# Kernel tuning notes

Hardware: AMD Instinct MI355X
Metric: run time of the kernel (lower is better)

The kernel has to match this reference:

```python
import jax, jax.numpy as jnp
from jax import lax
import numpy as np

N, E, G, CPG = 4096, 16, 14, 8  # wafers, experts, groups (wafer sub-arrays), channels per group
C = G * CPG  # 112


def setup_inputs() -> dict:
    key = jax.random.key(0)
    ks = jax.random.split(key, 9)
    s = 0.05
    x = jax.random.normal(ks[0], (N, G, 8, 8), jnp.float32)
    keys = jax.random.randint(ks[1], (N,), 0, E)
    # hexagonal wafer conv mask (buffer in the torch module); corners zeroed
    conv_mask = jnp.array([[1.0, 1.0, 0.0], [1.0, 1.0, 1.0], [0.0, 1.0, 1.0]], jnp.float32)
    enc_conv_w = jax.random.normal(ks[2], (E, C, 1, 3, 3), jnp.float32) * s
    enc_dense_w = jax.random.normal(ks[3], (E, G, 8, 128), jnp.float32) * s
    enc_dense_b = jax.random.normal(ks[4], (E, G, 8), jnp.float32) * s
    dec_dense_w = jax.random.normal(ks[5], (E, G, 128, 8), jnp.float32) * s
    dec_dense_b = jax.random.normal(ks[6], (E, G, 128), jnp.float32) * s
    dec_tconv_w = jax.random.normal(ks[7], (E, C, 1, 3, 3), jnp.float32) * s
    dec_tconv_b = jax.random.normal(ks[8], (E, G), jnp.float32) * s
    return dict(x=x, keys=keys, conv_mask=conv_mask,
                enc_conv_w=enc_conv_w, enc_dense_w=enc_dense_w, enc_dense_b=enc_dense_b,
                dec_dense_w=dec_dense_w, dec_dense_b=dec_dense_b,
                dec_tconv_w=dec_tconv_w, dec_tconv_b=dec_tconv_b)


def reference(x, keys, conv_mask, enc_conv_w, enc_dense_w, enc_dense_b,
              dec_dense_w, dec_dense_b, dec_tconv_w, dec_tconv_b):
    n = x.shape[0]
    dn = ('NCHW', 'OIHW', 'NCHW')

    # ---- encoder: masked grouped conv (bias=False) ----
    wc = enc_conv_w[keys] * conv_mask  # [N,112,1,3,3]; mask broadcasts over spatial taps

    def enc_conv(xi, wi):
        return lax.conv_general_dilated(xi[None], wi, (1, 1), 'SAME',
                                        feature_group_count=G, dimension_numbers=dn)[0]

    h = jax.nn.relu(jax.vmap(enc_conv)(x, wc))           # [N,112,8,8]
    h = h.reshape(n, C, 4, 2, 4, 2).max(axis=(3, 5))     # MaxPool2d(2) -> [N,112,4,4]
    feat = h.reshape(n, G, CPG * 16)                      # [N,14,128] (group-major, matches torch view)
    z = jax.nn.relu(jnp.einsum('ngof,ngf->ngo', enc_dense_w[keys], feat) + enc_dense_b[keys])  # [N,14,8]

    # ---- decoder ----
    y = jax.nn.relu(jnp.einsum('ngfo,ngo->ngf', dec_dense_w[keys], z) + dec_dense_b[keys])  # [N,14,128]
    y = y.reshape(n, C, 4, 4)

    # ConvTranspose2d(112,14,3,stride=2,pad=1,outpad=1,groups=14) as a dilated forward conv
    # with spatially flipped kernels: per group, 8 in -> 1 out.
    wt = jnp.flip(dec_tconv_w[keys].reshape(n, G, CPG, 3, 3), axis=(-2, -1))  # [N,14,8,3,3] OIHW
    bt = dec_tconv_b[keys]  # [N,14]

    def dec_tconv(yi, wi, bi):
        o = lax.conv_general_dilated(yi[None], wi, (1, 1), ((1, 2), (1, 2)),
                                     lhs_dilation=(2, 2), feature_group_count=G,
                                     dimension_numbers=dn)[0]
        return o + bi[:, None, None]

    out = jax.vmap(dec_tconv)(y, wt, bt)  # [N,14,8,8]
    return jax.nn.relu(out)
```

## Files before the change

kernel.cpp:

```cpp
#include <hip/hip_runtime.h>
#include <hip/hip_fp16.h>

#define NG 14
#define NE 16
#define NW 32
#define YW 152

typedef __fp16 h2 __attribute__((ext_vector_type(2)));
typedef __fp16 h4 __attribute__((ext_vector_type(4)));
typedef __fp16 h8 __attribute__((ext_vector_type(8)));

__device__ __forceinline__ float hdot4(h4 a, h4 b, float c) {
    const h2 a0 = __builtin_shufflevector(a, a, 0, 1);
    const h2 a1 = __builtin_shufflevector(a, a, 2, 3);
    const h2 b0 = __builtin_shufflevector(b, b, 0, 1);
    const h2 b1 = __builtin_shufflevector(b, b, 2, 3);
    return __builtin_amdgcn_fdot2(a1, b1, __builtin_amdgcn_fdot2(a0, b0, c, false), false);
}

__global__ __launch_bounds__(1024) void bin_kernel(const int* __restrict__ keys, int N,
                                                   int NBW, int* __restrict__ sorted) {
    __shared__ int hist[NE], offs[NE], cur[NE];
    __shared__ int runTot;
    const int t = threadIdx.x;
    if (t < NE) { hist[t] = 0; cur[t] = 0; }
    __syncthreads();
    for (int i = t; i < N; i += 1024) atomicAdd(&hist[keys[i]], 1);
    __syncthreads();
    if (t == 0) {
        int run = 0;
        for (int e = 0; e < NE; ++e) { offs[e] = run; run += (hist[e] + NW - 1) & ~(NW - 1); }
        runTot = run;
    }
    __syncthreads();
    for (int i = t; i < N; i += 1024) {
        const int e = keys[i];
        sorted[offs[e] + atomicAdd(&cur[e], 1)] = i;
    }
    {
        const int e = t >> 6, l = t & 63;
        const int cnt = hist[e];
        const int padded = (cnt + NW - 1) & ~(NW - 1);
        if (l < padded - cnt) sorted[offs[e] + cnt + l] = -1;
    }
    for (int i = runTot + t; i < NBW; i += 1024) sorted[i] = -1;
}

#define LOADROW(dst, R) do {                                  \
    const float4 a_ = *(const float4*)(xg + (R) * 8);         \
    const float4 b_ = *(const float4*)(xg + (R) * 8 + 4);     \
    dst[0]=0.f; dst[9]=0.f;                                   \
    dst[1]=a_.x; dst[2]=a_.y; dst[3]=a_.z; dst[4]=a_.w;       \
    dst[5]=b_.x; dst[6]=b_.y; dst[7]=b_.z; dst[8]=b_.w;       \
} while (0)

#define CONVGEMV(PR, RM, R0_, R1_, R2_, TZ, BZ)                                \
    {                                                                          \
        float res[4];                                                          \
        _Pragma("unroll")                                                      \
        for (int pc = 0; pc < 4; ++pc) {                                       \
            float mx = 0.f;                                                    \
            _Pragma("unroll")                                                  \
            for (int cl = 0; cl < 2; ++cl) {                                   \
                const int c = 2 * pc + cl;                                     \
                float s0 = w3*R0_[c] + w4*R0_[c+1] + w5*R0_[c+2]               \
                         + w7*R1_[c+1] + w8*R1_[c+2];                          \
                if (!(TZ)) s0 += w0*RM[c] + w1*RM[c+1];                        \
                float s1 = w0*R0_[c] + w1*R0_[c+1]                             \
                         + w3*R1_[c] + w4*R1_[c+1] + w5*R1_[c+2];              \
                if (!(BZ)) s1 += w7*R2_[c+1] + w8*R2_[c+2];                    \
                mx = fmaxf(mx, fmaxf(s0, s1));                                 \
            }                                                                  \
            res[pc] = mx;                                                      \
        }                                                                      \
        const h2 ra = __builtin_amdgcn_cvt_pkrtz(res[0], res[1]);              \
        const h2 rb = __builtin_amdgcn_cvt_pkrtz(res[2], res[3]);              \
        const h2* eb2 = &ews2[((PR) * 8 + ch) * 20];                           \
        _Pragma("unroll")                                                      \
        for (int q = 0; q < 4; ++q) {                                          \
            const h8 v = *(const h8*)(eb2 + q * 4);                            \
            const h2 a0 = __builtin_shufflevector(v, v, 0, 1);                 \
            const h2 a1 = __builtin_shufflevector(v, v, 2, 3);                 \
            const h2 b0 = __builtin_shufflevector(v, v, 4, 5);                 \
            const h2 b1 = __builtin_shufflevector(v, v, 6, 7);                 \
            part[2*q]   = __builtin_amdgcn_fdot2(rb, a1,                       \
                          __builtin_amdgcn_fdot2(ra, a0, part[2*q],   false), false); \
            part[2*q+1] = __builtin_amdgcn_fdot2(rb, b1,                       \
                          __builtin_amdgcn_fdot2(ra, b0, part[2*q+1], false), false); \
        }                                                                      \
    }

__global__ __launch_bounds__(256, 6) void ae_main(
    const float* __restrict__ x,
    const int*   __restrict__ keys,
    const float* __restrict__ conv_mask,
    const float* __restrict__ enc_conv_w,
    const float* __restrict__ enc_dense_w,
    const float* __restrict__ enc_dense_b,
    const float* __restrict__ dec_dense_w,
    const float* __restrict__ dec_dense_b,
    const float* __restrict__ dec_tconv_w,
    const float* __restrict__ dec_tconv_b,
    const int*   __restrict__ sorted,
    float* __restrict__ out)
{
    const int t = threadIdx.x;
    const int chunk = blockIdx.x / NG;
    const int g = blockIdx.x - chunk * NG;

    __shared__ __attribute__((aligned(16))) __half yt[NW * YW];
    __shared__ __attribute__((aligned(16))) h2 ews2[640];
    __shared__ __attribute__((aligned(16))) h2 dws2[512];
    __shared__ __attribute__((aligned(16))) h2 wtr2[48];
    __shared__ __attribute__((aligned(16))) float wcs[72];
    __shared__ float dbs[128];
    __shared__ float ebs[8];

    const int* chunkIds = sorted + chunk * NW;
    const int i0 = chunkIds[0];
    if (i0 < 0) return;
    const int k = keys[i0];

    const int w = t >> 3, ch = t & 7;
    const int idw = chunkIds[w];
    const int idr = (idw < 0) ? i0 : idw;

    const float* xg = x + (size_t)idr * 896 + g * 64;
    float rowA[10], rowB[10], rowC[10], rowD[10], rowE[10];
    LOADROW(rowA, 0);
    LOADROW(rowB, 1);
    LOADROW(rowC, 2);
    LOADROW(rowD, 4);

    const size_t wg1024 = (size_t)(k * NG + g) * 1024;
    {
        const float4 w4_ = *(const float4*)(enc_dense_w + wg1024 + 4 * t);
        const int o = t >> 5, c2 = (t >> 2) & 7, pr = t & 3;
        const int base = (pr * 8 + c2) * 20 + o * 2;
        ews2[base]     = __builtin_amdgcn_cvt_pkrtz(w4_.x, w4_.y);
        ews2[base + 1] = __builtin_amdgcn_cvt_pkrtz(w4_.z, w4_.w);
    }
    if (t < 128) {
        const float4 a = *(const float4*)(dec_dense_w + wg1024 + 8 * t);
        const float4 b = *(const float4*)(dec_dense_w + wg1024 + 8 * t + 4);
        const int c2 = t >> 4, p = t & 15;
        h2* dst = &dws2[(p * 8 + (c2 ^ (p & 7))) * 4];
        dst[0] = __builtin_amdgcn_cvt_pkrtz(a.x, a.y);
        dst[1] = __builtin_amdgcn_cvt_pkrtz(a.z, a.w);
        dst[2] = __builtin_amdgcn_cvt_pkrtz(b.x, b.y);
        dst[3] = __builtin_amdgcn_cvt_pkrtz(b.z, b.w);
    } else if (t < 200) {
        const int i = t - 128, c2 = i / 9, tap = i - c2 * 9;
        wcs[tap * 8 + c2] = enc_conv_w[(size_t)k * 1008 + (g * 8 + c2) * 9 + tap] * conv_mask[tap];
    } else if (t < 208) {
        ebs[t - 200] = enc_dense_b[(size_t)k * 112 + g * 8 + (t - 200)];
    } else if (t < 256) {
        const int i = t - 208, tap = i >> 2, j = i & 3;
        h2 v = (h2)(__fp16)0.f;
        if (tap < 9) {
            const float wa = dec_tconv_w[(size_t)k * 1008 + (g * 8 + 2*j) * 9 + tap];
            const float wb = dec_tconv_w[(size_t)k * 1008 + (g * 8 + 2*j + 1) * 9 + tap];
            v = __builtin_amdgcn_cvt_pkrtz(wa, wb);
        }
        wtr2[tap * 4 + j] = v;
    }
    if (t < 128) {
        dbs[(t & 15) * 8 + (t >> 4)] = dec_dense_b[(size_t)k * 1792 + g * 128 + t];
    }
    __syncthreads();

    const float w0 = wcs[0*8+ch], w1 = wcs[1*8+ch], w3 = wcs[3*8+ch], w4 = wcs[4*8+ch],
                w5 = wcs[5*8+ch], w7 = wcs[7*8+ch], w8 = wcs[8*8+ch];
    float part[8] = {0.f,0.f,0.f,0.f,0.f,0.f,0.f,0.f};

    CONVGEMV(0, rowA, rowA, rowB, rowC, 1, 0);
    LOADROW(rowE, 3);
    CONVGEMV(1, rowB, rowC, rowE, rowD, 0, 0);
    LOADROW(rowA, 5);
    LOADROW(rowB, 6);
    CONVGEMV(2, rowE, rowD, rowA, rowB, 0, 0);
    LOADROW(rowC, 7);
    CONVGEMV(3, rowA, rowB, rowC, rowC, 0, 1);

    float z[8];
    #pragma unroll
    for (int o = 0; o < 8; ++o) {
        float v = part[o];
        v += __shfl_xor(v, 1);
        v += __shfl_xor(v, 2);
        v += __shfl_xor(v, 4);
        z[o] = fmaxf(v + ebs[o], 0.f);
    }
    const h2 z01 = __builtin_amdgcn_cvt_pkrtz(z[0], z[1]);
    const h2 z23 = __builtin_amdgcn_cvt_pkrtz(z[2], z[3]);
    const h2 z45 = __builtin_amdgcn_cvt_pkrtz(z[4], z[5]);
    const h2 z67 = __builtin_amdgcn_cvt_pkrtz(z[6], z[7]);

    __half* yw_ = yt + w * YW;
    #pragma unroll
    for (int pp = 0; pp < 2; ++pp) {
        const int p = ch + pp * 8;
        const int px = p & 7;
        const float4 db0 = *(const float4*)(dbs + p * 8);
        const float4 db1 = *(const float4*)(dbs + p * 8 + 4);
        const float dbv[8] = {db0.x, db0.y, db0.z, db0.w, db1.x, db1.y, db1.z, db1.w};
        __fp16 yv[8];
        #pragma unroll
        for (int c = 0; c < 8; ++c) {
            const h8 v = *(const h8*)(&dws2[(p * 8 + (c ^ px)) * 4]);
            const h2 v0 = __builtin_shufflevector(v, v, 0, 1);
            const h2 v1 = __builtin_shufflevector(v, v, 2, 3);
            const h2 v2 = __builtin_shufflevector(v, v, 4, 5);
            const h2 v3 = __builtin_shufflevector(v, v, 6, 7);
            float acc = dbv[c];
            acc = __builtin_amdgcn_fdot2(z01, v0, acc, false);
            acc = __builtin_amdgcn_fdot2(z23, v1, acc, false);
            acc = __builtin_amdgcn_fdot2(z45, v2, acc, false);
            acc = __builtin_amdgcn_fdot2(z67, v3, acc, false);
            yv[c ^ px] = (__fp16)fmaxf(acc, 0.f);
        }
        h8 o8;
        #pragma unroll
        for (int c = 0; c < 8; ++c) o8[c] = yv[c ^ px];
        *(h8*)(yw_ + (p >> 2) * 40 + (p & 3) * 8) = o8;
    }
    asm volatile("s_waitcnt lgkmcnt(0)" ::: "memory");

    const int oi = ch;
    int iA, rA, iB, rB;
    if ((oi & 1) == 0) { iA = oi >> 1; rA = 3; iB = 0; rB = 9; }
    else { iA = (oi - 1) >> 1; rA = 6;
           if (oi < 7) { iB = (oi + 1) >> 1; rB = 0; } else { iB = 0; rB = 9; } }
    const float bias = dec_tconv_b[k * NG + g];
    const __fp16* ywh = (const __fp16*)(yt) + w * YW;

    h8 yAv[4], yBv[4];
    #pragma unroll
    for (int j = 0; j < 4; ++j) {
        yAv[j] = *(const h8*)(ywh + iA * 40 + j * 8);
        yBv[j] = *(const h8*)(ywh + iB * 40 + j * 8);
    }
    float acc[8] = {0.f,0.f,0.f,0.f,0.f,0.f,0.f,0.f};
    #pragma unroll
    for (int hc = 0; hc < 2; ++hc) {
        const h4 wA0 = *(const h4*)(wtr2 + (rA + 0) * 4 + hc * 2);
        const h4 wA1 = *(const h4*)(wtr2 + (rA + 1) * 4 + hc * 2);
        const h4 wA2 = *(const h4*)(wtr2 + (rA + 2) * 4 + hc * 2);
        const h4 wB0 = *(const h4*)(wtr2 + (rB + 0) * 4 + hc * 2);
        const h4 wB1 = *(const h4*)(wtr2 + (rB + 1) * 4 + hc * 2);
        const h4 wB2 = *(const h4*)(wtr2 + (rB + 2) * 4 + hc * 2);
        h4 yA[4], yB[4];
        #pragma unroll
        for (int j = 0; j < 4; ++j) {
            yA[j] = hc ? __builtin_shufflevector(yAv[j], yAv[j], 4, 5, 6, 7)
                       : __builtin_shufflevector(yAv[j], yAv[j], 0, 1, 2, 3);
            yB[j] = hc ? __builtin_shufflevector(yBv[j], yBv[j], 4, 5, 6, 7)
                       : __builtin_shufflevector(yBv[j], yBv[j], 0, 1, 2, 3);
        }
        acc[0] = hdot4(wB1, yB[0], hdot4(wA1, yA[0], acc[0]));
        acc[1] = hdot4(wB0, yB[1], hdot4(wB2, yB[0],
                 hdot4(wA0, yA[1], hdot4(wA2, yA[0], acc[1]))));
        acc[2] = hdot4(wB1, yB[1], hdot4(wA1, yA[1], acc[2]));
        acc[3] = hdot4(wB0, yB[2], hdot4(wB2, yB[1],
                 hdot4(wA0, yA[2], hdot4(wA2, yA[1], acc[3]))));
        acc[4] = hdot4(wB1, yB[2], hdot4(wA1, yA[2], acc[4]));
        acc[5] = hdot4(wB0, yB[3], hdot4(wB2, yB[2],
                 hdot4(wA0, yA[3], hdot4(wA2, yA[2], acc[5]))));
        acc[6] = hdot4(wB1, yB[3], hdot4(wA1, yA[3], acc[6]));
        acc[7] = hdot4(wB2, yB[3], hdot4(wA2, yA[3], acc[7]));
    }
    if (idw >= 0) {
        float* og = out + (size_t)idw * 896 + g * 64 + oi * 8;
        *(float4*)(og)     = make_float4(fmaxf(acc[0]+bias,0.f), fmaxf(acc[1]+bias,0.f),
                                         fmaxf(acc[2]+bias,0.f), fmaxf(acc[3]+bias,0.f));
        *(float4*)(og + 4) = make_float4(fmaxf(acc[4]+bias,0.f), fmaxf(acc[5]+bias,0.f),
                                         fmaxf(acc[6]+bias,0.f), fmaxf(acc[7]+bias,0.f));
    }
}

extern "C" void kernel_launch(void* const* d_in, const int* in_sizes, int n_in,
                              void* d_out, int out_size, void* d_ws, size_t ws_size,
                              hipStream_t stream) {
    const float* x            = (const float*)d_in[0];
    const int*   keys         = (const int*)d_in[1];
    const float* conv_mask    = (const float*)d_in[2];
    const float* enc_conv_w   = (const float*)d_in[3];
    const float* enc_dense_w  = (const float*)d_in[4];
    const float* enc_dense_b  = (const float*)d_in[5];
    const float* dec_dense_w  = (const float*)d_in[6];
    const float* dec_dense_b  = (const float*)d_in[7];
    const float* dec_tconv_w  = (const float*)d_in[8];
    const float* dec_tconv_b  = (const float*)d_in[9];
    float* out = (float*)d_out;

    const int N = in_sizes[0] / (NG * 64);
    const int CHUNKS = (N + NE * (NW - 1)) / NW + 1;
    int* sorted = (int*)d_ws;

    bin_kernel<<<1, 1024, 0, stream>>>(keys, N, CHUNKS * NW, sorted);
    ae_main<<<CHUNKS * NG, 256, 0, stream>>>(
        x, keys, conv_mask, enc_conv_w, enc_dense_w, enc_dense_b,
        dec_dense_w, dec_dense_b, dec_tconv_w, dec_tconv_b, sorted, out);
}
```

Baseline: 26.96 us.

## Process two sorted chunks per block and reuse expert weights across them

Each block now handles a pair of consecutive sorted chunks for one group instead of a single chunk, which halves the grid. The per-expert weight staging into shared memory is skipped when the second chunk has the same expert, and a barrier is added only when the expert changes. This is meant to cut redundant weight loads and conversions plus per-block launch and setup overhead. In exchange, the two chunks run one after the other inside a block, so there is less parallelism across the GPU and a longer critical path per block.

```diff
diff --git a/kernel.cpp b/kernel.cpp
--- a/kernel.cpp
+++ b/kernel.cpp
@@ -102,11 +102,12 @@
     const float* __restrict__ dec_tconv_w,
     const float* __restrict__ dec_tconv_b,
     const int*   __restrict__ sorted,
+    const int    CHUNKS,
     float* __restrict__ out)
 {
     const int t = threadIdx.x;
-    const int chunk = blockIdx.x / NG;
-    const int g = blockIdx.x - chunk * NG;
+    const int pair = blockIdx.x / NG;
+    const int g = blockIdx.x - pair * NG;
 
     __shared__ __attribute__((aligned(16))) __half yt[NW * YW];
     __shared__ __attribute__((aligned(16))) h2 ews2[640];
@@ -116,165 +117,175 @@
     __shared__ float dbs[128];
     __shared__ float ebs[8];
 
-    const int* chunkIds = sorted + chunk * NW;
-    const int i0 = chunkIds[0];
-    if (i0 < 0) return;
-    const int k = keys[i0];
-
     const int w = t >> 3, ch = t & 7;
-    const int idw = chunkIds[w];
-    const int idr = (idw < 0) ? i0 : idw;
-
-    const float* xg = x + (size_t)idr * 896 + g * 64;
     float rowA[10], rowB[10], rowC[10], rowD[10], rowE[10];
-    LOADROW(rowA, 0);
-    LOADROW(rowB, 1);
-    LOADROW(rowC, 2);
-    LOADROW(rowD, 4);
-
-    const size_t wg1024 = (size_t)(k * NG + g) * 1024;
-    {
-        const float4 w4_ = *(const float4*)(enc_dense_w + wg1024 + 4 * t);
-        const int o = t >> 5, c2 = (t >> 2) & 7, pr = t & 3;
-        const int base = (pr * 8 + c2) * 20 + o * 2;
-        ews2[base]     = __builtin_amdgcn_cvt_pkrtz(w4_.x, w4_.y);
-        ews2[base + 1] = __builtin_amdgcn_cvt_pkrtz(w4_.z, w4_.w);
-    }
-    if (t < 128) {
-        const float4 a = *(const float4*)(dec_dense_w + wg1024 + 8 * t);
-        const float4 b = *(const float4*)(dec_dense_w + wg1024 + 8 * t + 4);
-        const int c2 = t >> 4, p = t & 15;
-        h2* dst = &dws2[(p * 8 + (c2 ^ (p & 7))) * 4];
-        dst[0] = __builtin_amdgcn_cvt_pkrtz(a.x, a.y);
-        dst[1] = __builtin_amdgcn_cvt_pkrtz(a.z, a.w);
-        dst[2] = __builtin_amdgcn_cvt_pkrtz(b.x, b.y);
-        dst[3] = __builtin_amdgcn_cvt_pkrtz(b.z, b.w);
-    } else if (t < 200) {
-        const int i = t - 128, c2 = i / 9, tap = i - c2 * 9;
-        wcs[tap * 8 + c2] = enc_conv_w[(size_t)k * 1008 + (g * 8 + c2) * 9 + tap] * conv_mask[tap];
-    } else if (t < 208) {
-        ebs[t - 200] = enc_dense_b[(size_t)k * 112 + g * 8 + (t - 200)];
-    } else if (t < 256) {
-        const int i = t - 208, tap = i >> 2, j = i & 3;
-        h2 v = (h2)(__fp16)0.f;
-        if (tap < 9) {
-            const float wa = dec_tconv_w[(size_t)k * 1008 + (g * 8 + 2*j) * 9 + tap];
-            const float wb = dec_tconv_w[(size_t)k * 1008 + (g * 8 + 2*j + 1) * 9 + tap];
-            v = __builtin_amdgcn_cvt_pkrtz(wa, wb);
-        }
-        wtr2[tap * 4 + j] = v;
-    }
-    if (t < 128) {
-        dbs[(t & 15) * 8 + (t >> 4)] = dec_dense_b[(size_t)k * 1792 + g * 128 + t];
-    }
-    __syncthreads();
-
-    const float w0 = wcs[0*8+ch], w1 = wcs[1*8+ch], w3 = wcs[3*8+ch], w4 = wcs[4*8+ch],
-                w5 = wcs[5*8+ch], w7 = wcs[7*8+ch], w8 = wcs[8*8+ch];
-    float part[8] = {0.f,0.f,0.f,0.f,0.f,0.f,0.f,0.f};
-
-    CONVGEMV(0, rowA, rowA, rowB, rowC, 1, 0);
-    LOADROW(rowE, 3);
-    CONVGEMV(1, rowB, rowC, rowE, rowD, 0, 0);
-    LOADROW(rowA, 5);
-    LOADROW(rowB, 6);
-    CONVGEMV(2, rowE, rowD, rowA, rowB, 0, 0);
-    LOADROW(rowC, 7);
-    CONVGEMV(3, rowA, rowB, rowC, rowC, 0, 1);
-
-    float z[8];
-    #pragma unroll
-    for (int o = 0; o < 8; ++o) {
-        float v = part[o];
-        v += __shfl_xor(v, 1);
-        v += __shfl_xor(v, 2);
-        v += __shfl_xor(v, 4);
-        z[o] = fmaxf(v + ebs[o], 0.f);
-    }
-    const h2 z01 = __builtin_amdgcn_cvt_pkrtz(z[0], z[1]);
-    const h2 z23 = __builtin_amdgcn_cvt_pkrtz(z[2], z[3]);
-    const h2 z45 = __builtin_amdgcn_cvt_pkrtz(z[4], z[5]);
-    const h2 z67 = __builtin_amdgcn_cvt_pkrtz(z[6], z[7]);
-
-    __half* yw_ = yt + w * YW;
-    #pragma unroll
-    for (int pp = 0; pp < 2; ++pp) {
-        const int p = ch + pp * 8;
-        const int px = p & 7;
-        const float4 db0 = *(const float4*)(dbs + p * 8);
-        const float4 db1 = *(const float4*)(dbs + p * 8 + 4);
-        const float dbv[8] = {db0.x, db0.y, db0.z, db0.w, db1.x, db1.y, db1.z, db1.w};
-        __fp16 yv[8];
+    int kcur = -1;
+
+    for (int c2 = 0; c2 < 2; ++c2) {
+        const int chunk = pair * 2 + c2;
+        if (chunk >= CHUNKS) break;
+        const int* chunkIds = sorted + chunk * NW;
+        const int i0 = chunkIds[0];
+        if (i0 < 0) break;
+        const int k = keys[i0];
+
+        const int idw = chunkIds[w];
+        const int idr = (idw < 0) ? i0 : idw;
+        const float* xg = x + (size_t)idr * 896 + g * 64;
+
+        LOADROW(rowA, 0);
+        LOADROW(rowB, 1);
+        LOADROW(rowC, 2);
+        LOADROW(rowD, 4);
+
+        if (k != kcur) {
+            if (kcur >= 0) __syncthreads();
+            const size_t wg1024 = (size_t)(k * NG + g) * 1024;
+            {
+                const float4 w4_ = *(const float4*)(enc_dense_w + wg1024 + 4 * t);
+                const int o = t >> 5, cc = (t >> 2) & 7, pr = t & 3;
+                const int base = (pr * 8 + cc) * 20 + o * 2;
+                ews2[base]     = __builtin_amdgcn_cvt_pkrtz(w4_.x, w4_.y);
+                ews2[base + 1] = __builtin_amdgcn_cvt_pkrtz(w4_.z, w4_.w);
+            }
+            if (t < 128) {
+                const float4 a = *(const float4*)(dec_dense_w + wg1024 + 8 * t);
+                const float4 b = *(const float4*)(dec_dense_w + wg1024 + 8 * t + 4);
+                const int cc = t >> 4, p = t & 15;
+                h2* dst = &dws2[(p * 8 + (cc ^ (p & 7))) * 4];
+                dst[0] = __builtin_amdgcn_cvt_pkrtz(a.x, a.y);
+                dst[1] = __builtin_amdgcn_cvt_pkrtz(a.z, a.w);
+                dst[2] = __builtin_amdgcn_cvt_pkrtz(b.x, b.y);
+                dst[3] = __builtin_amdgcn_cvt_pkrtz(b.z, b.w);
+            } else if (t < 200) {
+                const int i = t - 128, cc = i / 9, tap = i - cc * 9;
+                wcs[tap * 8 + cc] = enc_conv_w[(size_t)k * 1008 + (g * 8 + cc) * 9 + tap] * conv_mask[tap];
+            } else if (t < 208) {
+                ebs[t - 200] = enc_dense_b[(size_t)k * 112 + g * 8 + (t - 200)];
+            } else if (t < 256) {
+                const int i = t - 208, tap = i >> 2, j = i & 3;
+                h2 v = (h2)(__fp16)0.f;
+                if (tap < 9) {
+                    const float wa = dec_tconv_w[(size_t)k * 1008 + (g * 8 + 2*j) * 9 + tap];
+                    const float wb = dec_tconv_w[(size_t)k * 1008 + (g * 8 + 2*j + 1) * 9 + tap];
+                    v = __builtin_amdgcn_cvt_pkrtz(wa, wb);
+                }
+                wtr2[tap * 4 + j] = v;
+            }
+            if (t < 128) {
+                dbs[(t & 15) * 8 + (t >> 4)] = dec_dense_b[(size_t)k * 1792 + g * 128 + t];
+            }
+            __syncthreads();
+            kcur = k;
+        }
+
+        const float w0 = wcs[0*8+ch], w1 = wcs[1*8+ch], w3 = wcs[3*8+ch], w4 = wcs[4*8+ch],
+                    w5 = wcs[5*8+ch], w7 = wcs[7*8+ch], w8 = wcs[8*8+ch];
+        float part[8] = {0.f,0.f,0.f,0.f,0.f,0.f,0.f,0.f};
+
+        CONVGEMV(0, rowA, rowA, rowB, rowC, 1, 0);
+        LOADROW(rowE, 3);
+        CONVGEMV(1, rowB, rowC, rowE, rowD, 0, 0);
+        LOADROW(rowA, 5);
+        LOADROW(rowB, 6);
+        CONVGEMV(2, rowE, rowD, rowA, rowB, 0, 0);
+        LOADROW(rowC, 7);
+        CONVGEMV(3, rowA, rowB, rowC, rowC, 0, 1);
+
+        float z[8];
         #pragma unroll
-        for (int c = 0; c < 8; ++c) {
-            const h8 v = *(const h8*)(&dws2[(p * 8 + (c ^ px)) * 4]);
-            const h2 v0 = __builtin_shufflevector(v, v, 0, 1);
-            const h2 v1 = __builtin_shufflevector(v, v, 2, 3);
-            const h2 v2 = __builtin_shufflevector(v, v, 4, 5);
-            const h2 v3 = __builtin_shufflevector(v, v, 6, 7);
-            float acc = dbv[c];
-            acc = __builtin_amdgcn_fdot2(z01, v0, acc, false);
-            acc = __builtin_amdgcn_fdot2(z23, v1, acc, false);
-            acc = __builtin_amdgcn_fdot2(z45, v2, acc, false);
-            acc = __builtin_amdgcn_fdot2(z67, v3, acc, false);
-            yv[c ^ px] = (__fp16)fmaxf(acc, 0.f);
-        }
-        h8 o8;
+        for (int o = 0; o < 8; ++o) {
+            float v = part[o];
+            v += __shfl_xor(v, 1);
+            v += __shfl_xor(v, 2);
+            v += __shfl_xor(v, 4);
+            z[o] = fmaxf(v + ebs[o], 0.f);
+        }
+        const h2 z01 = __builtin_amdgcn_cvt_pkrtz(z[0], z[1]);
+        const h2 z23 = __builtin_amdgcn_cvt_pkrtz(z[2], z[3]);
+        const h2 z45 = __builtin_amdgcn_cvt_pkrtz(z[4], z[5]);
+        const h2 z67 = __builtin_amdgcn_cvt_pkrtz(z[6], z[7]);
+
+        __half* yw_ = yt + w * YW;
         #pragma unroll
-        for (int c = 0; c < 8; ++c) o8[c] = yv[c ^ px];
-        *(h8*)(yw_ + (p >> 2) * 40 + (p & 3) * 8) = o8;
-    }
-    asm volatile("s_waitcnt lgkmcnt(0)" ::: "memory");
-
-    const int oi = ch;
-    int iA, rA, iB, rB;
-    if ((oi & 1) == 0) { iA = oi >> 1; rA = 3; iB = 0; rB = 9; }
-    else { iA = (oi - 1) >> 1; rA = 6;
-           if (oi < 7) { iB = (oi + 1) >> 1; rB = 0; } else { iB = 0; rB = 9; } }
-    const float bias = dec_tconv_b[k * NG + g];
-    const __fp16* ywh = (const __fp16*)(yt) + w * YW;
-
-    h8 yAv[4], yBv[4];
-    #pragma unroll
-    for (int j = 0; j < 4; ++j) {
-        yAv[j] = *(const h8*)(ywh + iA * 40 + j * 8);
-        yBv[j] = *(const h8*)(ywh + iB * 40 + j * 8);
-    }
-    float acc[8] = {0.f,0.f,0.f,0.f,0.f,0.f,0.f,0.f};
-    #pragma unroll
-    for (int hc = 0; hc < 2; ++hc) {
-        const h4 wA0 = *(const h4*)(wtr2 + (rA + 0) * 4 + hc * 2);
-        const h4 wA1 = *(const h4*)(wtr2 + (rA + 1) * 4 + hc * 2);
-        const h4 wA2 = *(const h4*)(wtr2 + (rA + 2) * 4 + hc * 2);
-        const h4 wB0 = *(const h4*)(wtr2 + (rB + 0) * 4 + hc * 2);
-        const h4 wB1 = *(const h4*)(wtr2 + (rB + 1) * 4 + hc * 2);
-        const h4 wB2 = *(const h4*)(wtr2 + (rB + 2) * 4 + hc * 2);
-        h4 yA[4], yB[4];
+        for (int pp = 0; pp < 2; ++pp) {
+            const int p = ch + pp * 8;
+            const int px = p & 7;
+            const float4 db0 = *(const float4*)(dbs + p * 8);
+            const float4 db1 = *(const float4*)(dbs + p * 8 + 4);
+            const float dbv[8] = {db0.x, db0.y, db0.z, db0.w, db1.x, db1.y, db1.z, db1.w};
+            __fp16 yv[8];
+            #pragma unroll
+            for (int c = 0; c < 8; ++c) {
+                const h8 v = *(const h8*)(&dws2[(p * 8 + (c ^ px)) * 4]);
+                const h2 v0 = __builtin_shufflevector(v, v, 0, 1);
+                const h2 v1 = __builtin_shufflevector(v, v, 2, 3);
+                const h2 v2 = __builtin_shufflevector(v, v, 4, 5);
+                const h2 v3 = __builtin_shufflevector(v, v, 6, 7);
+                float acc = dbv[c];
+                acc = __builtin_amdgcn_fdot2(z01, v0, acc, false);
+                acc = __builtin_amdgcn_fdot2(z23, v1, acc, false);
+                acc = __builtin_amdgcn_fdot2(z45, v2, acc, false);
+                acc = __builtin_amdgcn_fdot2(z67, v3, acc, false);
+                yv[c ^ px] = (__fp16)fmaxf(acc, 0.f);
+            }
+            h8 o8;
+            #pragma unroll
+            for (int c = 0; c < 8; ++c) o8[c] = yv[c ^ px];
+            *(h8*)(yw_ + (p >> 2) * 40 + (p & 3) * 8) = o8;
+        }
+        asm volatile("s_waitcnt lgkmcnt(0)" ::: "memory");
+
+        const int oi = ch;
+        int iA, rA, iB, rB;
+        if ((oi & 1) == 0) { iA = oi >> 1; rA = 3; iB = 0; rB = 9; }
+        else { iA = (oi - 1) >> 1; rA = 6;
+               if (oi < 7) { iB = (oi + 1) >> 1; rB = 0; } else { iB = 0; rB = 9; } }
+        const float bias = dec_tconv_b[k * NG + g];
+        const __fp16* ywh = (const __fp16*)(yt) + w * YW;
+
+        h8 yAv[4], yBv[4];
         #pragma unroll
         for (int j = 0; j < 4; ++j) {
-            yA[j] = hc ? __builtin_shufflevector(yAv[j], yAv[j], 4, 5, 6, 7)
-                       : __builtin_shufflevector(yAv[j], yAv[j], 0, 1, 2, 3);
-            yB[j] = hc ? __builtin_shufflevector(yBv[j], yBv[j], 4, 5, 6, 7)
-                       : __builtin_shufflevector(yBv[j], yBv[j], 0, 1, 2, 3);
-        }
-        acc[0] = hdot4(wB1, yB[0], hdot4(wA1, yA[0], acc[0]));
-        acc[1] = hdot4(wB0, yB[1], hdot4(wB2, yB[0],
-                 hdot4(wA0, yA[1], hdot4(wA2, yA[0], acc[1]))));
-        acc[2] = hdot4(wB1, yB[1], hdot4(wA1, yA[1], acc[2]));
-        acc[3] = hdot4(wB0, yB[2], hdot4(wB2, yB[1],
-                 hdot4(wA0, yA[2], hdot4(wA2, yA[1], acc[3]))));
-        acc[4] = hdot4(wB1, yB[2], hdot4(wA1, yA[2], acc[4]));
-        acc[5] = hdot4(wB0, yB[3], hdot4(wB2, yB[2],
-                 hdot4(wA0, yA[3], hdot4(wA2, yA[2], acc[5]))));
-        acc[6] = hdot4(wB1, yB[3], hdot4(wA1, yA[3], acc[6]));
-        acc[7] = hdot4(wB2, yB[3], hdot4(wA2, yA[3], acc[7]));
-    }
-    if (idw >= 0) {
-        float* og = out + (size_t)idw * 896 + g * 64 + oi * 8;
-        *(float4*)(og)     = make_float4(fmaxf(acc[0]+bias,0.f), fmaxf(acc[1]+bias,0.f),
-                                         fmaxf(acc[2]+bias,0.f), fmaxf(acc[3]+bias,0.f));
-        *(float4*)(og + 4) = make_float4(fmaxf(acc[4]+bias,0.f), fmaxf(acc[5]+bias,0.f),
-                                         fmaxf(acc[6]+bias,0.f), fmaxf(acc[7]+bias,0.f));
+            yAv[j] = *(const h8*)(ywh + iA * 40 + j * 8);
+            yBv[j] = *(const h8*)(ywh + iB * 40 + j * 8);
+        }
+        float acc[8] = {0.f,0.f,0.f,0.f,0.f,0.f,0.f,0.f};
+        #pragma unroll
+        for (int hc = 0; hc < 2; ++hc) {
+            const h4 wA0 = *(const h4*)(wtr2 + (rA + 0) * 4 + hc * 2);
+            const h4 wA1 = *(const h4*)(wtr2 + (rA + 1) * 4 + hc * 2);
+            const h4 wA2 = *(const h4*)(wtr2 + (rA + 2) * 4 + hc * 2);
+            const h4 wB0 = *(const h4*)(wtr2 + (rB + 0) * 4 + hc * 2);
+            const h4 wB1 = *(const h4*)(wtr2 + (rB + 1) * 4 + hc * 2);
+            const h4 wB2 = *(const h4*)(wtr2 + (rB + 2) * 4 + hc * 2);
+            h4 yA[4], yB[4];
+            #pragma unroll
+            for (int j = 0; j < 4; ++j) {
+                yA[j] = hc ? __builtin_shufflevector(yAv[j], yAv[j], 4, 5, 6, 7)
+                           : __builtin_shufflevector(yAv[j], yAv[j], 0, 1, 2, 3);
+                yB[j] = hc ? __builtin_shufflevector(yBv[j], yBv[j], 4, 5, 6, 7)
+                           : __builtin_shufflevector(yBv[j], yBv[j], 0, 1, 2, 3);
+            }
+            acc[0] = hdot4(wB1, yB[0], hdot4(wA1, yA[0], acc[0]));
+            acc[1] = hdot4(wB0, yB[1], hdot4(wB2, yB[0],
+                     hdot4(wA0, yA[1], hdot4(wA2, yA[0], acc[1]))));
+            acc[2] = hdot4(wB1, yB[1], hdot4(wA1, yA[1], acc[2]));
+            acc[3] = hdot4(wB0, yB[2], hdot4(wB2, yB[1],
+                     hdot4(wA0, yA[2], hdot4(wA2, yA[1], acc[3]))));
+            acc[4] = hdot4(wB1, yB[2], hdot4(wA1, yA[2], acc[4]));
+            acc[5] = hdot4(wB0, yB[3], hdot4(wB2, yB[2],
+                     hdot4(wA0, yA[3], hdot4(wA2, yA[2], acc[5]))));
+            acc[6] = hdot4(wB1, yB[3], hdot4(wA1, yA[3], acc[6]));
+            acc[7] = hdot4(wB2, yB[3], hdot4(wA2, yA[3], acc[7]));
+        }
+        if (idw >= 0) {
+            float* og = out + (size_t)idw * 896 + g * 64 + oi * 8;
+            *(float4*)(og)     = make_float4(fmaxf(acc[0]+bias,0.f), fmaxf(acc[1]+bias,0.f),
+                                             fmaxf(acc[2]+bias,0.f), fmaxf(acc[3]+bias,0.f));
+            *(float4*)(og + 4) = make_float4(fmaxf(acc[4]+bias,0.f), fmaxf(acc[5]+bias,0.f),
+                                             fmaxf(acc[6]+bias,0.f), fmaxf(acc[7]+bias,0.f));
+        }
     }
 }
 
@@ -295,10 +306,11 @@
 
     const int N = in_sizes[0] / (NG * 64);
     const int CHUNKS = (N + NE * (NW - 1)) / NW + 1;
+    const int NPAIRS = (CHUNKS + 1) / 2;
     int* sorted = (int*)d_ws;
 
     bin_kernel<<<1, 1024, 0, stream>>>(keys, N, CHUNKS * NW, sorted);
-    ae_main<<<CHUNKS * NG, 256, 0, stream>>>(
+    ae_main<<<NPAIRS * NG, 256, 0, stream>>>(
         x, keys, conv_mask, enc_conv_w, enc_dense_w, enc_dense_b,
-        dec_dense_w, dec_dense_b, dec_tconv_w, dec_tconv_b, sorted, out);
+        dec_dense_w, dec_dense_b, dec_tconv_w, dec_tconv_b, sorted, CHUNKS, out);
 }
```

Measured after the change: 50.84 us. 1.89x slower.
